# Optimization experiments

Hardware: AMD Instinct MI355X
Metric: run time of the kernel (lower is better)

Reference implementation:

```python
import jax, jax.numpy as jnp
import numpy as np

IN_F, OUT_F = 4096, 14336
F8_MAX = 448.0  # max magnitude of float8_e4m3fn


def setup_inputs() -> dict:
    key = jax.random.key(0)
    kx, kw, kb = jax.random.split(key, 3)
    x = jax.random.normal(kx, (2, 512, IN_F), dtype=jnp.bfloat16)
    w = jax.random.normal(kw, (OUT_F, IN_F), dtype=jnp.float32) * 0.02
    # per-tensor scale: amax / 448 (as in F8Linear.__init__)
    w_scale = (jnp.maximum(jnp.abs(w).max(), 1e-30) / F8_MAX).astype(jnp.float32)
    # quantize to fp8 e4m3; roundtrip back to float32 so the stored values are
    # exactly the fp8-representable values (float32 container keeps the bwd
    # reference's jax.vjp happy while the math is identical)
    w_f8 = jnp.clip(w / w_scale, -F8_MAX, F8_MAX).astype(jnp.float8_e4m3fn).astype(jnp.float32)
    bias = jax.random.normal(kb, (OUT_F,), dtype=jnp.float32) * 0.02
    return {"x": x, "weight_f8": w_f8, "w_scale": w_scale, "bias": bias}


def reference(x, weight_f8, w_scale, bias):
    # dequantize to activation dtype, then GEMM: y = x @ w^T + b
    w = weight_f8.astype(x.dtype) * w_scale.astype(x.dtype)   # [out, in]
    y = jnp.einsum('bsi,oi->bso', x, w) + bias.astype(x.dtype)
    return y
```

## Files before the change

kernel.cpp:

```cpp
#include <hip/hip_runtime.h>
#include <hip/hip_bf16.h>
#include <stdint.h>


#define IN_F   4096
#define OUT_F  14336
#define M_TOT  1024

#define BM 128
#define BN 128

#define TM 256
#define TN 256
#define TK 64
#define KT8 (IN_F / TK)

typedef __bf16  bf16x8 __attribute__((ext_vector_type(8)));
typedef __bf16  bf16x4 __attribute__((ext_vector_type(4)));
typedef float   f32x4  __attribute__((ext_vector_type(4)));

__device__ __forceinline__ void async_copy16(const void* g, void* l) {
    __builtin_amdgcn_global_load_lds(
        (const __attribute__((address_space(1))) void*)g,
        (__attribute__((address_space(3))) void*)l,
        16, 0, 0);
}

__global__ void detect_x_dtype(const uint32_t* __restrict__ xb,
                               int* __restrict__ flag) {
    __shared__ int any_low;
    if (threadIdx.x == 0) any_low = 0;
    __syncthreads();
    uint32_t bad = 0;
    for (int i = threadIdx.x; i < 1024; i += 256) bad |= (xb[i] & 0xFFFFu);
    if (bad) atomicOr(&any_low, 1);
    __syncthreads();
    if (threadIdx.x == 0) *flag = (any_low == 0) ? 1 : 0;
}

__global__ __launch_bounds__(256) void cvt_x_kernel(
    const void* __restrict__ xraw, bf16x8* __restrict__ out,
    const int* __restrict__ flag) {
    const int f32w = (*flag != 0);
    const int i = blockIdx.x * 256 + threadIdx.x;
    if (f32w) {
        const f32x4* in = (const f32x4*)xraw;
        f32x4 a = in[2 * i];
        f32x4 b = in[2 * i + 1];
        bf16x8 o;
        o[0] = (__bf16)a[0]; o[1] = (__bf16)a[1];
        o[2] = (__bf16)a[2]; o[3] = (__bf16)a[3];
        o[4] = (__bf16)b[0]; o[5] = (__bf16)b[1];
        o[6] = (__bf16)b[2]; o[7] = (__bf16)b[3];
        out[i] = o;
    } else {
        out[i] = ((const bf16x8*)xraw)[i];
    }
}

__global__ __launch_bounds__(512, 2) void gemm_fused_8ph(
    const __bf16* __restrict__ xb,
    const float*  __restrict__ wf,
    const float*  __restrict__ w_scale,
    const float*  __restrict__ bias,
    void*         __restrict__ yraw,
    const int*    __restrict__ flag_p)
{
    __shared__ __align__(16) __bf16 As[2][2][128 * TK];
    __shared__ __align__(16) __bf16 Bs[2][2][128 * TK];

    const int f32w = (*flag_p != 0);
    const int t    = threadIdx.x;
    const int lane = t & 63;
    const int wv   = t >> 6;
    const int wm   = wv >> 2;
    const int wn   = wv & 3;
    const int lidx = lane & 15;
    const int q    = lane >> 4;

    const int flat = blockIdx.x;
    const int xcd  = flat & 7;
    const int slot = flat >> 3;
    const int ni   = xcd * 7 + (slot >> 2);
    const int mi   = slot & 3;
    const int m0   = mi * TM;
    const int n0   = ni * TN;

    const float scale = w_scale[0];

    const __bf16* gA = xb + (size_t)m0 * IN_F;

    int srow[2], scgl[2];
    #pragma unroll
    for (int i = 0; i < 2; ++i) {
        const int s = i * 512 + t;
        srow[i] = s >> 3;
        scgl[i] = (s & 7) ^ (srow[i] & 7);
    }

    const float* gB0 = wf + (size_t)(n0 + srow[0]) * IN_F + scgl[0] * 8;
    const float* gB1 = wf + (size_t)(n0 + srow[1]) * IN_F + scgl[1] * 8;

    int aoff[4][2], boff[2][2];
    #pragma unroll
    for (int qm = 0; qm < 4; ++qm) {
        const int row = qm * 32 + wm * 16 + lidx;
        #pragma unroll
        for (int kg = 0; kg < 2; ++kg)
            aoff[qm][kg] = row * 128 + (((kg * 4 + q) ^ (row & 7)) * 16);
    }
    #pragma unroll
    for (int qn = 0; qn < 2; ++qn) {
        const int row = qn * 64 + wn * 16 + lidx;
        #pragma unroll
        for (int kg = 0; kg < 2; ++kg)
            boff[qn][kg] = row * 128 + (((kg * 4 + q) ^ (row & 7)) * 16);
    }

    const f32x4 zero4 = {0.f, 0.f, 0.f, 0.f};
    f32x4 acc[8][4];
    #pragma unroll
    for (int i = 0; i < 8; ++i)
        #pragma unroll
        for (int j = 0; j < 4; ++j)
            acc[i][j] = zero4;

    bf16x8 areg[4][2], breg[2][2];
    f32x4  Br0[4], Br1[4];

#define STAGE_A(tile, half) do {                                              \
    __bf16* _dst = &As[(tile) & 1][(half)][0];                                \
    const __bf16* _src = gA + (size_t)(half) * 128 * IN_F + (tile) * TK;      \
    async_copy16(_src + (size_t)srow[0] * IN_F + scgl[0] * 8, _dst + t * 8);  \
    async_copy16(_src + (size_t)srow[1] * IN_F + scgl[1] * 8,                 \
                 _dst + (512 + t) * 8);                                       \
} while (0)

#define B_LOAD(tile, half, Rv) do {                                           \
    const float* _p0 = gB0 + (size_t)(half) * 128 * IN_F + (tile) * TK;       \
    const float* _p1 = gB1 + (size_t)(half) * 128 * IN_F + (tile) * TK;       \
    Rv[0] = *(const f32x4*)_p0;                                               \
    Rv[1] = *(const f32x4*)(_p0 + 4);                                         \
    Rv[2] = *(const f32x4*)_p1;                                               \
    Rv[3] = *(const f32x4*)(_p1 + 4);                                         \
} while (0)

#define B_WRITE(tile, half, Rv) do {                                          \
    __bf16* _d = &Bs[(tile) & 1][(half)][0];                                  \
    bf16x8 _o;                                                                \
    _o[0] = (__bf16)Rv[0][0]; _o[1] = (__bf16)Rv[0][1];                       \
    _o[2] = (__bf16)Rv[0][2]; _o[3] = (__bf16)Rv[0][3];                       \
    _o[4] = (__bf16)Rv[1][0]; _o[5] = (__bf16)Rv[1][1];                       \
    _o[6] = (__bf16)Rv[1][2]; _o[7] = (__bf16)Rv[1][3];                       \
    *(bf16x8*)(_d + (size_t)t * 8) = _o;                                      \
    _o[0] = (__bf16)Rv[2][0]; _o[1] = (__bf16)Rv[2][1];                       \
    _o[2] = (__bf16)Rv[2][2]; _o[3] = (__bf16)Rv[2][3];                       \
    _o[4] = (__bf16)Rv[3][0]; _o[5] = (__bf16)Rv[3][1];                       \
    _o[6] = (__bf16)Rv[3][2]; _o[7] = (__bf16)Rv[3][3];                       \
    *(bf16x8*)(_d + (size_t)(512 + t) * 8) = _o;                              \
} while (0)

#define LOAD_A(base) do {                                                     \
    _Pragma("unroll")                                                         \
    for (int _qm = 0; _qm < 4; ++_qm) {                                       \
        areg[_qm][0] = *(const bf16x8*)((base) + aoff[_qm][0]);               \
        areg[_qm][1] = *(const bf16x8*)((base) + aoff[_qm][1]);               \
    }                                                                         \
} while (0)

#define LOAD_B(base) do {                                                     \
    _Pragma("unroll")                                                         \
    for (int _qn = 0; _qn < 2; ++_qn) {                                       \
        breg[_qn][0] = *(const bf16x8*)((base) + boff[_qn][0]);               \
        breg[_qn][1] = *(const bf16x8*)((base) + boff[_qn][1]);               \
    }                                                                         \
} while (0)

#define MFMA16(MO, NO) do {                                                   \
    __builtin_amdgcn_s_setprio(1);                                            \
    _Pragma("unroll")                                                         \
    for (int _qm = 0; _qm < 4; ++_qm)                                         \
        _Pragma("unroll")                                                     \
        for (int _qn = 0; _qn < 2; ++_qn) {                                   \
            acc[(MO) + _qm][(NO) + _qn] =                                     \
                __builtin_amdgcn_mfma_f32_16x16x32_bf16(                      \
                    areg[_qm][0], breg[_qn][0], acc[(MO) + _qm][(NO) + _qn],  \
                    0, 0, 0);                                                 \
            acc[(MO) + _qm][(NO) + _qn] =                                     \
                __builtin_amdgcn_mfma_f32_16x16x32_bf16(                      \
                    areg[_qm][1], breg[_qn][1], acc[(MO) + _qm][(NO) + _qn],  \
                    0, 0, 0);                                                 \
        }                                                                     \
    __builtin_amdgcn_s_setprio(0);                                            \
} while (0)

#define BARR() __builtin_amdgcn_s_barrier()
#define LGKM0() do {                                                          \
    asm volatile("s_waitcnt lgkmcnt(0)" ::: "memory");                        \
    __builtin_amdgcn_sched_barrier(0);                                        \
} while (0)
#define VMCNT(n) asm volatile("s_waitcnt vmcnt(" #n ")" ::: "memory")

    B_LOAD(0, 0, Br0);
    B_LOAD(0, 1, Br1);
    STAGE_A(0, 0);
    STAGE_A(0, 1);
    STAGE_A(1, 0);
    VMCNT(6);
    B_WRITE(0, 0, Br0);
    B_WRITE(0, 1, Br1);
    VMCNT(2);
    LGKM0();
    BARR();

    for (int kt = 0; kt < KT8; ++kt) {
        const char* a0 = (const char*)&As[kt & 1][0][0];
        const char* a1 = (const char*)&As[kt & 1][1][0];
        const char* b0 = (const char*)&Bs[kt & 1][0][0];
        const char* b1 = (const char*)&Bs[kt & 1][1][0];

        LOAD_A(a0);
        LOAD_B(b0);
        if (kt + 1 < KT8) B_LOAD(kt + 1, 0, Br0);
        BARR(); LGKM0();
        MFMA16(0, 0);
        BARR();

        LOAD_B(b1);
        if (kt + 1 < KT8) {
            B_LOAD(kt + 1, 1, Br1);
            STAGE_A(kt + 1, 1);
        }
        BARR(); LGKM0();
        MFMA16(0, 2);
        BARR();

        LOAD_A(a1);
        if (kt + 1 < KT8) {
            VMCNT(6);
            B_WRITE(kt + 1, 0, Br0);
        }
        if (kt + 2 < KT8) STAGE_A(kt + 2, 0);
        BARR(); LGKM0();
        MFMA16(4, 2);
        BARR();

        LOAD_B(b0);
        if (kt + 1 < KT8) {
            if (kt + 2 < KT8) { VMCNT(4); } else { VMCNT(2); }
            B_WRITE(kt + 1, 1, Br1);
        }
        BARR(); LGKM0();
        MFMA16(4, 0);
        if (kt + 1 < KT8) {
            if (kt + 2 < KT8) { VMCNT(2); } else { VMCNT(0); }
        }
        BARR();
    }

#undef STAGE_A
#undef B_LOAD
#undef B_WRITE
#undef LOAD_A
#undef LOAD_B
#undef MFMA16
#undef BARR
#undef LGKM0
#undef VMCNT

    float bv[4];
    #pragma unroll
    for (int nf = 0; nf < 4; ++nf)
        bv[nf] = bias[n0 + (nf >> 1) * 128 + (nf & 1) * 64 + wn * 16 + lidx];

    if (f32w) {
        float* yf = (float*)yraw;
        #pragma unroll
        for (int mf = 0; mf < 8; ++mf)
            #pragma unroll
            for (int r = 0; r < 4; ++r) {
                const int m = m0 + (mf >> 2) * 128 + (mf & 3) * 32 + wm * 16 + q * 4 + r;
                float* yp = yf + (size_t)m * OUT_F + n0 + wn * 16 + lidx;
                #pragma unroll
                for (int nf = 0; nf < 4; ++nf)
                    yp[(nf >> 1) * 128 + (nf & 1) * 64] =
                        acc[mf][nf][r] * scale + bv[nf];
            }
    } else {
        __bf16* yh = (__bf16*)yraw;
        #pragma unroll
        for (int mf = 0; mf < 8; ++mf)
            #pragma unroll
            for (int r = 0; r < 4; ++r) {
                const int m = m0 + (mf >> 2) * 128 + (mf & 3) * 32 + wm * 16 + q * 4 + r;
                __bf16* yp = yh + (size_t)m * OUT_F + n0 + wn * 16 + lidx;
                #pragma unroll
                for (int nf = 0; nf < 4; ++nf)
                    yp[(nf >> 1) * 128 + (nf & 1) * 64] =
                        (__bf16)(acc[mf][nf][r] * scale + bv[nf]);
            }
    }
}

__global__ __launch_bounds__(256) void f8linear_fallback(
    const void*  __restrict__ xraw,
    const float* __restrict__ wq,
    const float* __restrict__ w_scale,
    const float* __restrict__ bias,
    void*        __restrict__ yraw,
    const int*   __restrict__ flag_p)
{
    __shared__ __align__(16) __bf16 As[BM * 40];
    __shared__ __align__(16) __bf16 Bs[BN * 40];

    const int f32w = (*flag_p != 0);
    const int t    = threadIdx.x;
    const int lane = t & 63;
    const int wv   = t >> 6;
    const int wm   = wv >> 1;
    const int wn   = wv & 1;
    const int lidx = lane & 15;
    const int q    = lane >> 4;

    const int flat = blockIdx.x;
    const int xcd  = flat & 7;
    const int slot = flat >> 3;
    const int ni   = xcd * 14 + (slot >> 3);
    const int mi   = slot & 7;
    const int m0   = mi * BM;
    const int n0   = ni * BN;

    const float scale = w_scale[0];
    const float*  xf = (const float*)xraw;
    const __bf16* xh = (const __bf16*)xraw;

    const int af_row = t >> 3;
    const int af_col = (t & 7) * 4;
    int ah_row[2], ah_cg[2];
    #pragma unroll
    for (int i = 0; i < 2; ++i) {
        const int s = i * 256 + t;
        ah_row[i] = s >> 2;
        ah_cg[i]  = s & 3;
    }
    const int b_row = t >> 3;
    const int b_col = (t & 7) * 4;

    const f32x4 zero4 = {0.f, 0.f, 0.f, 0.f};
    f32x4 acc[4][4];
    #pragma unroll
    for (int i = 0; i < 4; ++i)
        #pragma unroll
        for (int j = 0; j < 4; ++j)
            acc[i][j] = zero4;

    f32x4  aregf[4];
    bf16x8 aregh[2];
    f32x4  breg[4];
    if (f32w) {
        #pragma unroll
        for (int i = 0; i < 4; ++i)
            aregf[i] = *reinterpret_cast<const f32x4*>(
                xf + (size_t)(m0 + af_row + i * 32) * IN_F + af_col);
    } else {
        #pragma unroll
        for (int i = 0; i < 2; ++i)
            aregh[i] = *reinterpret_cast<const bf16x8*>(
                xh + (size_t)(m0 + ah_row[i]) * IN_F + ah_cg[i] * 8);
    }
    #pragma unroll
    for (int i = 0; i < 4; ++i)
        breg[i] = *reinterpret_cast<const f32x4*>(
            wq + (size_t)(n0 + i * 32 + b_row) * IN_F + b_col);

    for (int kt = 0; kt < 128; ++kt) {
        const int k0 = kt * 32;
        if (f32w) {
            #pragma unroll
            for (int i = 0; i < 4; ++i) {
                bf16x4 pk;
                pk[0] = (__bf16)aregf[i][0];
                pk[1] = (__bf16)aregf[i][1];
                pk[2] = (__bf16)aregf[i][2];
                pk[3] = (__bf16)aregf[i][3];
                *reinterpret_cast<bf16x4*>(As + (af_row + i * 32) * 40 + af_col) = pk;
            }
        } else {
            #pragma unroll
            for (int i = 0; i < 2; ++i)
                *reinterpret_cast<bf16x8*>(As + ah_row[i] * 40 + ah_cg[i] * 8) = aregh[i];
        }
        #pragma unroll
        for (int i = 0; i < 4; ++i) {
            bf16x4 pk;
            pk[0] = (__bf16)breg[i][0];
            pk[1] = (__bf16)breg[i][1];
            pk[2] = (__bf16)breg[i][2];
            pk[3] = (__bf16)breg[i][3];
            *reinterpret_cast<bf16x4*>(Bs + (i * 32 + b_row) * 40 + b_col) = pk;
        }
        __syncthreads();
        if (kt + 1 < 128) {
            const int k1 = k0 + 32;
            if (f32w) {
                #pragma unroll
                for (int i = 0; i < 4; ++i)
                    aregf[i] = *reinterpret_cast<const f32x4*>(
                        xf + (size_t)(m0 + af_row + i * 32) * IN_F + k1 + af_col);
            } else {
                #pragma unroll
                for (int i = 0; i < 2; ++i)
                    aregh[i] = *reinterpret_cast<const bf16x8*>(
                        xh + (size_t)(m0 + ah_row[i]) * IN_F + k1 + ah_cg[i] * 8);
            }
            #pragma unroll
            for (int i = 0; i < 4; ++i)
                breg[i] = *reinterpret_cast<const f32x4*>(
                    wq + (size_t)(n0 + i * 32 + b_row) * IN_F + k1 + b_col);
        }
        bf16x8 afr[4], bfr[4];
        #pragma unroll
        for (int mt = 0; mt < 4; ++mt) {
            const int row = wm * 64 + mt * 16 + lidx;
            afr[mt] = *reinterpret_cast<const bf16x8*>(As + row * 40 + q * 8);
        }
        #pragma unroll
        for (int nt = 0; nt < 4; ++nt) {
            const int row = wn * 64 + nt * 16 + lidx;
            bfr[nt] = *reinterpret_cast<const bf16x8*>(Bs + row * 40 + q * 8);
        }
        #pragma unroll
        for (int mt = 0; mt < 4; ++mt)
            #pragma unroll
            for (int nt = 0; nt < 4; ++nt)
                acc[mt][nt] = __builtin_amdgcn_mfma_f32_16x16x32_bf16(
                    afr[mt], bfr[nt], acc[mt][nt], 0, 0, 0);
        __syncthreads();
    }

    float bv[4];
    #pragma unroll
    for (int nt = 0; nt < 4; ++nt)
        bv[nt] = bias[n0 + wn * 64 + nt * 16 + lidx];

    if (f32w) {
        float* yf = (float*)yraw;
        #pragma unroll
        for (int mt = 0; mt < 4; ++mt)
            #pragma unroll
            for (int r = 0; r < 4; ++r) {
                const int m = m0 + wm * 64 + mt * 16 + q * 4 + r;
                float* yp = yf + (size_t)m * OUT_F + n0 + wn * 64 + lidx;
                #pragma unroll
                for (int nt = 0; nt < 4; ++nt)
                    yp[nt * 16] = acc[mt][nt][r] * scale + bv[nt];
            }
    } else {
        __bf16* yh = (__bf16*)yraw;
        #pragma unroll
        for (int mt = 0; mt < 4; ++mt)
            #pragma unroll
            for (int r = 0; r < 4; ++r) {
                const int m = m0 + wm * 64 + mt * 16 + q * 4 + r;
                __bf16* yp = yh + (size_t)m * OUT_F + n0 + wn * 64 + lidx;
                #pragma unroll
                for (int nt = 0; nt < 4; ++nt)
                    yp[nt * 16] = (__bf16)(acc[mt][nt][r] * scale + bv[nt]);
            }
    }
}

extern "C" void kernel_launch(void* const* d_in, const int* in_sizes, int n_in,
                              void* d_out, int out_size, void* d_ws, size_t ws_size,
                              hipStream_t stream) {
    const void* px = nullptr; const void* pw = nullptr;
    const void* ps = nullptr; const void* pb = nullptr;
    for (int i = 0; i < n_in; ++i) {
        const long sz = in_sizes[i];
        if      (sz == (long)M_TOT * IN_F) px = d_in[i];
        else if (sz == (long)OUT_F * IN_F) pw = d_in[i];
        else if (sz == 1)                  ps = d_in[i];
        else if (sz == OUT_F)              pb = d_in[i];
    }
    if (!px) px = d_in[0];
    if (!pw) pw = d_in[1];
    if (!ps) ps = d_in[2];
    if (!pb) pb = d_in[3];

    const size_t X_BYTES  = (size_t)M_TOT * IN_F * 2;
    const size_t FLAG_OFF = X_BYTES;

    if (ws_size >= FLAG_OFF + 16) {
        __bf16* xbf  = (__bf16*)d_ws;
        int*    flag = (int*)((char*)d_ws + FLAG_OFF);

        const int grid8 = (M_TOT / TM) * (OUT_F / TN);

        detect_x_dtype<<<1, 256, 0, stream>>>((const uint32_t*)px, flag);
        cvt_x_kernel<<<2048, 256, 0, stream>>>(px, (bf16x8*)xbf, flag);
        gemm_fused_8ph<<<grid8, 512, 0, stream>>>(
            xbf, (const float*)pw, (const float*)ps, (const float*)pb,
            d_out, flag);
    } else {
        int* flag = (int*)d_ws;
        const int grid = (M_TOT / BM) * (OUT_F / BN);
        detect_x_dtype<<<1, 256, 0, stream>>>((const uint32_t*)px, flag);
        f8linear_fallback<<<grid, 256, 0, stream>>>(
            px, (const float*)pw, (const float*)ps, (const float*)pb, d_out, flag);
    }
}
```

Baseline: 506.4 us.

## Deepen B prefetch to two tiles ahead with ping-pong register sets

```diff
diff --git a/kernel.cpp b/kernel.cpp
--- a/kernel.cpp
+++ b/kernel.cpp
@@ -126,10 +126,10 @@
             acc[i][j] = zero4;
 
     bf16x8 areg[4][2], breg[2][2];
-    f32x4  Br0[4], Br1[4];
-
-#define STAGE_A(tile, half) do {                                              \
-    __bf16* _dst = &As[(tile) & 1][(half)][0];                                \
+    f32x4 RaE[4], RbE[4], RaO[4], RbO[4];
+
+#define STAGE_A(tile, half, BI) do {                                          \
+    __bf16* _dst = &As[(BI)][(half)][0];                                      \
     const __bf16* _src = gA + (size_t)(half) * 128 * IN_F + (tile) * TK;      \
     async_copy16(_src + (size_t)srow[0] * IN_F + scgl[0] * 8, _dst + t * 8);  \
     async_copy16(_src + (size_t)srow[1] * IN_F + scgl[1] * 8,                 \
@@ -145,8 +145,8 @@
     Rv[3] = *(const f32x4*)(_p1 + 4);                                         \
 } while (0)
 
-#define B_WRITE(tile, half, Rv) do {                                          \
-    __bf16* _d = &Bs[(tile) & 1][(half)][0];                                  \
+#define B_WRITE(half, BI, Rv) do {                                            \
+    __bf16* _d = &Bs[(BI)][(half)][0];                                        \
     bf16x8 _o;                                                                \
     _o[0] = (__bf16)Rv[0][0]; _o[1] = (__bf16)Rv[0][1];                       \
     _o[2] = (__bf16)Rv[0][2]; _o[3] = (__bf16)Rv[0][3];                       \
@@ -194,70 +194,70 @@
     __builtin_amdgcn_s_setprio(0);                                            \
 } while (0)
 
-#define BARR() __builtin_amdgcn_s_barrier()
-#define LGKM0() do {                                                          \
-    asm volatile("s_waitcnt lgkmcnt(0)" ::: "memory");                        \
-    __builtin_amdgcn_sched_barrier(0);                                        \
-} while (0)
-#define VMCNT(n) asm volatile("s_waitcnt vmcnt(" #n ")" ::: "memory")
-
-    B_LOAD(0, 0, Br0);
-    B_LOAD(0, 1, Br1);
-    STAGE_A(0, 0);
-    STAGE_A(0, 1);
-    STAGE_A(1, 0);
+#define BARR()    __builtin_amdgcn_s_barrier()
+#define LGKM0()   asm volatile("s_waitcnt lgkmcnt(0)" ::: "memory")
+#define VMCNT(n)  asm volatile("s_waitcnt vmcnt(" #n ")" ::: "memory")
+
+    B_LOAD(0, 0, RaE);
+    B_LOAD(0, 1, RbE);
+    STAGE_A(0, 0, 0);
+    STAGE_A(0, 1, 0);
+    VMCNT(4);
+    B_WRITE(0, 0, RaE);
+    B_WRITE(1, 0, RbE);
+    B_LOAD(1, 0, RaO);
+    B_LOAD(1, 1, RbO);
+    STAGE_A(1, 0, 1);
     VMCNT(6);
-    B_WRITE(0, 0, Br0);
-    B_WRITE(0, 1, Br1);
-    VMCNT(2);
     LGKM0();
     BARR();
 
-    for (int kt = 0; kt < KT8; ++kt) {
-        const char* a0 = (const char*)&As[kt & 1][0][0];
-        const char* a1 = (const char*)&As[kt & 1][1][0];
-        const char* b0 = (const char*)&Bs[kt & 1][0][0];
-        const char* b1 = (const char*)&Bs[kt & 1][1][0];
-
-        LOAD_A(a0);
-        LOAD_B(b0);
-        if (kt + 1 < KT8) B_LOAD(kt + 1, 0, Br0);
-        BARR(); LGKM0();
-        MFMA16(0, 0);
-        BARR();
-
-        LOAD_B(b1);
-        if (kt + 1 < KT8) {
-            B_LOAD(kt + 1, 1, Br1);
-            STAGE_A(kt + 1, 1);
-        }
-        BARR(); LGKM0();
-        MFMA16(0, 2);
-        BARR();
-
-        LOAD_A(a1);
-        if (kt + 1 < KT8) {
-            VMCNT(6);
-            B_WRITE(kt + 1, 0, Br0);
-        }
-        if (kt + 2 < KT8) STAGE_A(kt + 2, 0);
-        BARR(); LGKM0();
-        MFMA16(4, 2);
-        BARR();
-
-        LOAD_B(b0);
-        if (kt + 1 < KT8) {
-            if (kt + 2 < KT8) { VMCNT(4); } else { VMCNT(2); }
-            B_WRITE(kt + 1, 1, Br1);
-        }
-        BARR(); LGKM0();
-        MFMA16(4, 0);
-        if (kt + 1 < KT8) {
-            if (kt + 2 < KT8) { VMCNT(2); } else { VMCNT(0); }
-        }
-        BARR();
-    }
-
+#define TILE_BODY(kt, P, QI, RWa, RWb, LDa, LDb) do {                         \
+    const char* _a0 = (const char*)&As[(P)][0][0];                            \
+    const char* _a1 = (const char*)&As[(P)][1][0];                            \
+    const char* _b0 = (const char*)&Bs[(P)][0][0];                            \
+    const char* _b1 = (const char*)&Bs[(P)][1][0];                            \
+                   \
+    LOAD_A(_a0);                                                              \
+    LOAD_B(_b0);                                                              \
+    if ((kt) + 2 < KT8) B_LOAD((kt) + 2, 0, LDa);                             \
+    if ((kt) + 1 < KT8) STAGE_A((kt) + 1, 1, QI);                             \
+    BARR(); LGKM0();                                                          \
+    MFMA16(0, 0);                                                             \
+    BARR();                                                                   \
+                                    \
+    LOAD_B(_b1);                                                              \
+    if ((kt) + 2 < KT8) B_LOAD((kt) + 2, 1, LDb);                             \
+    BARR(); LGKM0();                                                          \
+    MFMA16(0, 2);                                                             \
+    BARR();                                                                   \
+          \
+          \
+          \
+    LOAD_A(_a1);                                                              \
+    if ((kt) + 1 < KT8) B_WRITE(0, QI, RWa);                                  \
+    if ((kt) + 2 < KT8) STAGE_A((kt) + 2, 0, P);                              \
+    LGKM0();                  \
+    BARR();                                                                   \
+    MFMA16(4, 2);                                                             \
+    BARR();                                                                   \
+                                    \
+    LOAD_B(_b0);                                                              \
+    if ((kt) + 1 < KT8) B_WRITE(1, QI, RWb);                                  \
+    LGKM0();                                                                  \
+    BARR();                                                                   \
+    MFMA16(4, 0);                                                             \
+    if ((kt) < KT8 - 2) { VMCNT(6); } else { VMCNT(0); }                      \
+    BARR();                                                                   \
+} while (0)
+
+    for (int it = 0; it < KT8 / 2; ++it) {
+        const int kte = 2 * it;
+        TILE_BODY(kte,     0, 1, RaO, RbO, RaE, RbE);
+        TILE_BODY(kte + 1, 1, 0, RaE, RbE, RaO, RbO);
+    }
+
+#undef TILE_BODY
 #undef STAGE_A
 #undef B_LOAD
 #undef B_WRITE
```

Measured after the change: 578.2 us. 1.14x slower.
